# Kernel optimization log

Hardware: AMD Instinct MI355X
Metric: run time of the kernel (lower is better)

The kernel has to match this reference:

```python
import jax, jax.numpy as jnp
import numpy as np

H, C = 5, 128          # heads, hidden_channels
NUM_GRAPHS = 500
N_NODES, N_EDGES = 20000, 320000


def gat_layer(x, edge_attr, src, dst, W, We, a_src, a_dst, a_edge, b):
    """PyG GATConv with edge_dim, add_self_loops=True, fill_value='mean', concat heads."""
    N = x.shape[0]
    ed = edge_attr.dtype
    # self-loop edge_attr = scatter-mean of incoming edge_attr per target node
    deg = jax.ops.segment_sum(jnp.ones((dst.shape[0],), ed), dst, num_segments=N)
    loop_attr = jax.ops.segment_sum(edge_attr, dst, num_segments=N) / jnp.maximum(deg, 1.0)[:, None]
    loop = jnp.arange(N, dtype=src.dtype)
    s = jnp.concatenate([src, loop])
    d = jnp.concatenate([dst, loop])
    ea = jnp.concatenate([edge_attr, loop_attr], axis=0)
    h = (x @ W).reshape(N, H, C)            # [N,H,C]
    e = (ea @ We).reshape(-1, H, C)         # [E2,H,C]
    a_l = (h * a_src).sum(-1)               # [N,H]
    a_r = (h * a_dst).sum(-1)               # [N,H]
    a_e = (e * a_edge).sum(-1)              # [E2,H]
    alpha = jax.nn.leaky_relu(a_l[s] + a_r[d] + a_e, 0.2)
    # segment softmax over destination neighborhoods
    amax = jax.ops.segment_max(alpha, d, num_segments=N)
    ex = jnp.exp(alpha - amax[d])
    denom = jax.ops.segment_sum(ex, d, num_segments=N)
    att = ex / (denom[d] + 1e-16)           # [E2,H]
    msg = h[s] * att[..., None]             # [E2,H,C]
    out = jax.ops.segment_sum(msg, d, num_segments=N).reshape(N, H * C)
    return out + b


def setup_inputs() -> dict:
    key = jax.random.key(0)
    ks = jax.random.split(key, 24)
    p = lambda k, sh: (jax.random.normal(k, sh, dtype=jnp.float32) * 0.05)
    inp = {
        "x": jax.random.normal(ks[0], (N_NODES, 43), dtype=jnp.float32),
        "edge_attr": jax.random.normal(ks[1], (N_EDGES, 10), dtype=jnp.float32),
        "W1": p(ks[2], (43, H * C)),   "We1": p(ks[3], (10, H * C)),
        "asrc1": p(ks[4], (H, C)), "adst1": p(ks[5], (H, C)), "aedge1": p(ks[6], (H, C)),
        "b1": jnp.zeros((H * C,), jnp.float32),
        "W2": p(ks[7], (H * C, H * C)), "We2": p(ks[8], (10, H * C)),
        "asrc2": p(ks[9], (H, C)), "adst2": p(ks[10], (H, C)), "aedge2": p(ks[11], (H, C)),
        "b2": jnp.zeros((H * C,), jnp.float32),
        "W3": p(ks[12], (H * C, H * C)), "We3": p(ks[13], (10, H * C)),
        "asrc3": p(ks[14], (H, C)), "adst3": p(ks[15], (H, C)), "aedge3": p(ks[16], (H, C)),
        "b3": jnp.zeros((H * C,), jnp.float32),
        "Wlin": p(ks[17], (H * C, 1)), "blin": jnp.zeros((1,), jnp.float32),
        "edge_index": jax.random.randint(ks[18], (2, N_EDGES), 0, N_NODES, dtype=jnp.int32),
        "batch": jnp.sort(jax.random.randint(ks[19], (N_NODES,), 0, NUM_GRAPHS, dtype=jnp.int32)),
    }
    return inp


def reference(x, edge_attr, W1, We1, asrc1, adst1, aedge1, b1,
              W2, We2, asrc2, adst2, aedge2, b2,
              W3, We3, asrc3, adst3, aedge3, b3,
              Wlin, blin, edge_index, batch):
    src, dst = edge_index[0], edge_index[1]
    h = jax.nn.relu(gat_layer(x, edge_attr, src, dst, W1, We1, asrc1, adst1, aedge1, b1))
    h = jax.nn.relu(gat_layer(h, edge_attr, src, dst, W2, We2, asrc2, adst2, aedge2, b2))
    h = gat_layer(h, edge_attr, src, dst, W3, We3, asrc3, adst3, aedge3, b3)
    # global mean pool over graphs
    cnt = jax.ops.segment_sum(jnp.ones((h.shape[0],), h.dtype), batch, num_segments=NUM_GRAPHS)
    pooled = jax.ops.segment_sum(h, batch, num_segments=NUM_GRAPHS) / jnp.maximum(cnt, 1.0)[:, None]
    return (pooled @ Wlin + blin).squeeze(-1)   # [NUM_GRAPHS]
```

## Files before the change

kernel.cpp:

```cpp
#include <hip/hip_runtime.h>

#define N_NODESC 20000
#define N_EDGESC 320000
#define HC 640
#define NGRAPH 500

typedef unsigned short u16;
typedef unsigned int u32;
typedef __attribute__((ext_vector_type(8))) short bf16x8;
typedef __attribute__((ext_vector_type(4))) float f32x4;

__device__ __forceinline__ float wred_sum(float v){
  #pragma unroll
  for(int o=32;o;o>>=1) v += __shfl_xor(v,o,64);
  return v;
}
__device__ __forceinline__ float lrelu(float x){ return x>0.f? x:0.2f*x; }

__device__ __forceinline__ u16 f2bf(float f){
  u32 u=__float_as_uint(f);
  u32 r=u+0x7FFFu+((u>>16)&1u);
  return (u16)(r>>16);
}
__device__ __forceinline__ float bf2f(u16 s){ return __uint_as_float(((u32)s)<<16); }
__device__ __forceinline__ float bflo(u32 w){ return __uint_as_float(w<<16); }
__device__ __forceinline__ float bfhi(u32 w){ return __uint_as_float(w&0xFFFF0000u); }

__device__ __forceinline__ void gload16(const void* g, void* l){
  __builtin_amdgcn_global_load_lds((const __attribute__((address_space(1))) void*)g,
                                   (__attribute__((address_space(3))) void*)l, 16, 0, 0);
}

__device__ __forceinline__ size_t fidx(int r, int k, int KB){
  return ((size_t)(r>>4)*KB + (k>>5))*512 + (((k>>3)&3)*16 + (r&15))*8 + (k&7);
}


__global__ void k_count(const int* __restrict__ dst, int* __restrict__ cnt){
  int i=blockIdx.x*blockDim.x+threadIdx.x;
  if(i>=N_EDGESC) return;
  atomicAdd(&cnt[dst[i]],1);
}

__global__ void k_scan(const int* __restrict__ cnt, int* __restrict__ rptr, int* __restrict__ pos){
  __shared__ int ps[1024];
  int t=threadIdx.x;
  const int CH=20;
  int beg=t*CH, end=min(beg+CH, N_NODESC);
  int s=0;
  for(int i=beg;i<end;i++) s+=cnt[i];
  ps[t]=s; __syncthreads();
  for(int off=1;off<1024;off<<=1){
    int v=(t>=off)? ps[t-off]:0;
    __syncthreads();
    ps[t]+=v;
    __syncthreads();
  }
  int base=ps[t]-s;
  for(int i=beg;i<end;i++){ rptr[i]=base; pos[i]=base; base+=cnt[i]; }
}

__global__ void k_scatter(const int* __restrict__ dst, const int* __restrict__ src,
                          const float* __restrict__ eattr, int* __restrict__ pos,
                          int* __restrict__ srcE, int* __restrict__ dstC,
                          float* __restrict__ eattrC){
  int i=blockIdx.x*blockDim.x+threadIdx.x;
  if(i>=N_EDGESC) return;
  int d=dst[i];
  int j=atomicAdd(&pos[d],1);
  dstC[j]=d;
  srcE[j]=src[i];
  const float* ep=&eattr[(size_t)i*10];
  float* op=&eattrC[(size_t)j*10];
  #pragma unroll
  for(int k=0;k<10;k++) op[k]=ep[k];
}

__global__ __launch_bounds__(256) void k_loop_attr(const float* __restrict__ eattrC,
    const int* __restrict__ rptr, const int* __restrict__ cnt,
    float* __restrict__ lattr){
  int tid=threadIdx.x, lane=tid&63;
  int n=blockIdx.x*4+(tid>>6);
  if(n>=N_NODESC) return;
  int beg=rptr[n], deg=cnt[n];
  float s[10]={0,0,0,0,0,0,0,0,0,0};
  for(int off=lane; off<deg; off+=64){
    const float* ep=&eattrC[(size_t)(beg+off)*10];
    #pragma unroll
    for(int k=0;k<10;k++) s[k]+=ep[k];
  }
  float inv=1.f/fmaxf((float)deg,1.f);
  #pragma unroll
  for(int k=0;k<10;k++){
    float tot=wred_sum(s[k]);
    if(lane==0) lattr[(size_t)n*10+k]=tot*inv;
  }
}


__global__ void k_padxb(const float* __restrict__ x, u16* __restrict__ xb){
  int idx=blockIdx.x*blockDim.x+threadIdx.x;
  if(idx>=N_NODESC*64) return;
  int n=idx>>6, kk=idx&63;
  float v = kk<43 ? x[n*43+kk] : 0.f;
  xb[idx]=f2bf(v);
}

__global__ void k_conv_w3(const float* __restrict__ W0, const float* __restrict__ W1,
                          const float* __restrict__ W2,
                          u16* __restrict__ hi, u16* __restrict__ lo){
  const int R0=HC*64, R1=R0+HC*HC;
  const int TOT=R1+HC*HC;
  int idx=blockIdx.x*blockDim.x+threadIdx.x;
  if(idx>=TOT) return;
  const float* W; int local, KP, KL, base;
  if(idx<R0){ W=W0; local=idx; KP=64; KL=43; base=0; }
  else if(idx<R1){ W=W1; local=idx-R0; KP=HC; KL=HC; base=R0; }
  else { W=W2; local=idx-R1; KP=HC; KL=HC; base=R1; }
  int n=local/KP, kk=local-n*KP;
  float v = kk<KL ? W[(size_t)kk*HC+n] : 0.f;
  u16 h=f2bf(v);
  size_t off=(size_t)base + fidx(n,kk,KP>>5);
  hi[off]=h;
  lo[off]=f2bf(v-bf2f(h));
}


__global__ void k_ve3(const float* __restrict__ We0, const float* __restrict__ ae0,
                      const float* __restrict__ We1, const float* __restrict__ ae1,
                      const float* __restrict__ We2, const float* __restrict__ ae2,
                      float* __restrict__ ve3){
  int t=threadIdx.x;
  if(t>=150) return;
  int L=t/50, r=t-50*L, k=r/5, h=r%5;
  const float* We = (L==0)?We0:(L==1)?We1:We2;
  const float* ae = (L==0)?ae0:(L==1)?ae1:ae2;
  float s=0.f;
  for(int c=0;c<128;c++) s += We[k*HC + h*128 + c]*ae[h*128+c];
  ve3[t]=s;
}

__global__ void k_vs0(const float* __restrict__ W0, const float* __restrict__ asrc,
                      const float* __restrict__ adst,
                      const float* __restrict__ bias2, const float* __restrict__ wlin,
                      float* __restrict__ VS, float* __restrict__ VD,
                      float* __restrict__ cb){
  int t=threadIdx.x;
  if(t<320){
    int k=t/5, h=t%5;
    float sv=0.f, dv=0.f;
    if(k<43){
      for(int c=0;c<128;c++){
        float wv=W0[(size_t)k*HC + h*128 + c];
        sv+=wv*asrc[h*128+c];
        dv+=wv*adst[h*128+c];
      }
    }
    VS[t]=sv; VD[t]=dv;
  }else{
    int lane=t-320;
    float s=0.f;
    for(int c=lane;c<HC;c+=64) s+=bias2[c]*wlin[c];
    s=wred_sum(s);
    if(lane==0) cb[0]=s;
  }
}

__global__ void k_vq2(const float* __restrict__ W2, const float* __restrict__ asrc,
                      const float* __restrict__ adst, const float* __restrict__ wlin,
                      float* __restrict__ V2){
  int t=blockIdx.x*blockDim.x+threadIdx.x;
  if(t>=HC*15) return;
  int k=t/15, o=t-15*k;
  int h=o%5, grp=o/5;
  const float* v = (grp==0)? asrc : (grp==1)? adst : wlin;
  const float* wr=&W2[(size_t)k*HC + h*128];
  const float* vr=&v[h*128];
  float s=0.f;
  for(int c=0;c<128;c++) s+=wr[c]*vr[c];
  V2[t]=s;
}

__global__ __launch_bounds__(256) void k_alar0(const float* __restrict__ x,
    const float* __restrict__ VS, const float* __restrict__ VD,
    float* __restrict__ al, float* __restrict__ ar){
  __shared__ float vs[320], vd[320];
  if(threadIdx.x<320){ vs[threadIdx.x]=VS[threadIdx.x]; vd[threadIdx.x]=VD[threadIdx.x]; }
  __syncthreads();
  int idx=blockIdx.x*blockDim.x+threadIdx.x;
  if(idx>=N_NODESC*5) return;
  int n=idx/5, h=idx-5*n;
  float sa=0.f, sd=0.f;
  const float* xr=&x[(size_t)n*43];
  for(int k=0;k<43;k++){
    float xv=xr[k];
    sa+=xv*vs[k*5+h];
    sd+=xv*vd[k*5+h];
  }
  al[idx]=sa; ar[idx]=sd;
}

__global__ __launch_bounds__(256) void k_edge_terms3(const float* __restrict__ eattrC,
    const float* __restrict__ lattr, const float* __restrict__ ve3,
    float* __restrict__ aeC3, float* __restrict__ ael3){
  __shared__ float ves[150];
  if(threadIdx.x<150) ves[threadIdx.x]=ve3[threadIdx.x];
  __syncthreads();
  const int NEDGET=N_EDGESC+N_NODESC*5;
  int idx=blockIdx.x*blockDim.x+threadIdx.x;
  if(idx>=3*NEDGET) return;
  int L=idx/NEDGET, r=idx-L*NEDGET;
  const float* vl=&ves[L*50];
  if(r<N_EDGESC){
    float ev[10];
    const float* ep=&eattrC[(size_t)r*10];
    #pragma unroll
    for(int k=0;k<10;k++) ev[k]=ep[k];
    #pragma unroll
    for(int hh=0;hh<5;hh++){
      float s=0.f;
      #pragma unroll
      for(int k=0;k<10;k++) s+=ev[k]*vl[k*5+hh];
      aeC3[(size_t)L*N_EDGESC*5 + (size_t)r*5+hh]=s;
    }
  }else{
    int t=r-N_EDGESC;
    int n=t/5, h=t-5*n;
    float s=0.f;
    #pragma unroll
    for(int k=0;k<10;k++) s+=lattr[(size_t)n*10+k]*vl[k*5+h];
    ael3[(size_t)L*N_NODESC*5 + t]=s;
  }
}

__global__ void k_edgew(const int* __restrict__ srcE, const int* __restrict__ dstC,
                        const float* __restrict__ al, const float* __restrict__ ar,
                        const float* __restrict__ aeC, float* __restrict__ wE){
  int j=blockIdx.x*blockDim.x+threadIdx.x;
  if(j>=N_EDGESC) return;
  int s=srcE[j], d=dstC[j];
  const float* av=&aeC[(size_t)j*5];
  float* wp=&wE[(size_t)j*5];
  #pragma unroll
  for(int h=0;h<5;h++)
    wp[h]=__expf(lrelu(al[s*5+h]+ar[d*5+h]+av[h]));
}


__global__ __launch_bounds__(256) void k_aggx(const u16* __restrict__ xb,
    const int* __restrict__ srcE, const int* __restrict__ rptr, const int* __restrict__ cnt,
    const float* __restrict__ al, const float* __restrict__ ar, const float* __restrict__ ael,
    const float* __restrict__ wE,
    u16* __restrict__ aggx, float* __restrict__ den0){
  const size_t HSZ=(size_t)N_NODESC*64;
  int tid=threadIdx.x, lane=tid&63;
  int n=blockIdx.x*4+(tid>>6);
  if(n>=N_NODESC) return;
  float den[5], acc[5];
  #pragma unroll
  for(int h=0;h<5;h++)
    den[h]=__expf(lrelu(al[n*5+h]+ar[n*5+h]+ael[n*5+h]));
  float xn=bf2f(xb[(size_t)n*64+lane]);
  #pragma unroll
  for(int h=0;h<5;h++) acc[h]=den[h]*xn;
  int beg=rptr[n], end=beg+cnt[n];
  int j=beg;
  for(; j+7<end; j+=8){
    int sj[8]; float xv[8];
    #pragma unroll
    for(int u=0;u<8;u++) sj[u]=srcE[j+u];
    #pragma unroll
    for(int u=0;u<8;u++) xv[u]=bf2f(xb[(size_t)sj[u]*64+lane]);
    #pragma unroll
    for(int u=0;u<8;u++){
      const float* wp=&wE[(size_t)(j+u)*5];
      #pragma unroll
      for(int h=0;h<5;h++){
        float w=wp[h];
        den[h]+=w;
        acc[h]+=w*xv[u];
      }
    }
  }
  for(; j<end; j++){
    int sj=srcE[j];
    float xv=bf2f(xb[(size_t)sj*64+lane]);
    const float* wp=&wE[(size_t)j*5];
    #pragma unroll
    for(int h=0;h<5;h++){
      float w=wp[h];
      den[h]+=w;
      acc[h]+=w*xv;
    }
  }
  size_t fo=fidx(n,lane,2);
  #pragma unroll
  for(int h=0;h<5;h++) aggx[(size_t)h*HSZ+fo]=f2bf(acc[h]);
  if(lane<5) den0[(size_t)n*5+lane]=den[lane];
}

__global__ __launch_bounds__(256,3) void k_gemm_l0b(
    const u16* __restrict__ AGX,
    const u16* __restrict__ Bhi, const u16* __restrict__ Blo,
    const float* __restrict__ den0, const float* __restrict__ bias,
    u16* __restrict__ A1, int M, int nblk){
  const size_t HSZ=(size_t)N_NODESC*64;
  __shared__ u16 lds[2*3*4096];
  int tid=threadIdx.x;
  int lane=tid&63;
  int w=tid>>6;
  int l15=lane&15, lg=lane>>4;
  int orig=blockIdx.x;
  int q=nblk>>3, r=nblk&7;
  int xcd=orig&7, off=orig>>3;
  int wg=(xcd<r? xcd*(q+1) : r*(q+1)+(xcd-r)*q)+off;
  int by=wg/5, bx=wg-5*by;
  int row0=by*128, col0=bx*128;
  int wr=w>>1, wc=w&1;
  const u16* A=AGX+(size_t)bx*HSZ;

  f32x4 zero = {0.f,0.f,0.f,0.f};
  f32x4 acc[4][4];
  #pragma unroll
  for(int i=0;i<4;i++)
    #pragma unroll
    for(int j=0;j<4;j++) acc[i][j]=zero;

  auto stage=[&](int b, int k0){
    u16* base = lds + b*3*4096;
    int kb=k0>>5;
    #pragma unroll
    for(int c=0;c<2;c++){
      int sb=w+4*c;
      size_t af=((size_t)((row0>>4)+sb)*2 + kb)*512 + lane*8;
      size_t bf=((size_t)((col0>>4)+sb)*2 + kb)*512 + lane*8;
      gload16(A+af, base + sb*512);
      gload16(Bhi+bf, base+4096 + sb*512);
      gload16(Blo+bf, base+8192 + sb*512);
    }
  };

  stage(0,0);
  __syncthreads();
  int cur=0;
  for(int t=0;t<2;t++){
    if(t==0) stage(1,32);
    u16* cb = lds + cur*3*4096;
    bf16x8 ah[4], bh[4], bl[4];
    #pragma unroll
    for(int i=0;i<4;i++){
      ah[i]=*(const bf16x8*)&cb[(wr*4+i)*512 + lane*8];
      bh[i]=*(const bf16x8*)&cb[4096+(wc*4+i)*512 + lane*8];
      bl[i]=*(const bf16x8*)&cb[8192+(wc*4+i)*512 + lane*8];
    }
    #pragma unroll
    for(int i=0;i<4;i++)
      #pragma unroll
      for(int j=0;j<4;j++){
        acc[i][j]=__builtin_amdgcn_mfma_f32_16x16x32_bf16(ah[i],bh[j],acc[i][j],0,0,0);
        acc[i][j]=__builtin_amdgcn_mfma_f32_16x16x32_bf16(ah[i],bl[j],acc[i][j],0,0,0);
      }
    __syncthreads();
    cur^=1;
  }

  #pragma unroll
  for(int i=0;i<4;i++){
    #pragma unroll
    for(int j=0;j<4;j++){
      int col=col0+wc*64+j*16+l15;
      float bv=bias[col];
      #pragma unroll
      for(int rr=0;rr<4;rr++){
        int row=row0+wr*64+i*16+lg*4+rr;
        if(row<M){
          float dv=den0[(size_t)row*5+bx];
          float v=acc[i][j][rr]/(dv+1e-16f)+bv;
          v=fmaxf(v,0.f);
          A1[fidx(row,col,20)]=f2bf(v);
        }
      }
    }
  }
}


__global__ __launch_bounds__(256,3) void k_gemm64(
    const u16* __restrict__ A,
    const u16* __restrict__ B,
    const float* __restrict__ asrc, const float* __restrict__ adst,
    u16* __restrict__ hb, float* __restrict__ al, float* __restrict__ ar,
    int M, int KP, int nblk){
  __shared__ u16 lds[4*6144];
  int tid=threadIdx.x;
  int lane=tid&63;
  int w=tid>>6;
  int l15=lane&15, lg=lane>>4;
  int orig=blockIdx.x;
  int q=nblk>>3, r=nblk&7;
  int xcd=orig&7, off=orig>>3;
  int wg=(xcd<r? xcd*(q+1) : r*(q+1)+(xcd-r)*q)+off;
  int by=wg/5, bx=wg-5*by;
  int row0=by*64, col0=bx*128;
  int KB=KP>>5;

  f32x4 zero = {0.f,0.f,0.f,0.f};
  f32x4 acc[4][2];
  #pragma unroll
  for(int i=0;i<4;i++){ acc[i][0]=zero; acc[i][1]=zero; }

  auto stage=[&](int b, int k0){
    u16* base = lds + b*6144;
    int kb=k0>>5;
    size_t af=((size_t)((row0>>4)+w)*KB + kb)*512 + lane*8;
    gload16(A+af, base + w*512);
    #pragma unroll
    for(int c=0;c<2;c++){
      int sb=w+4*c;
      size_t bf=((size_t)((col0>>4)+sb)*KB + kb)*512 + lane*8;
      gload16(B+bf, base+2048 + sb*512);
    }
  };

  int nt=KP/32;
  stage(0,0);
  stage(1,32);
  for(int t=0;t<nt;t++){
    int nb=t+2;
    if(nb<nt) stage(nb&3, nb*32);
    if(nb<nt)      { asm volatile("s_waitcnt vmcnt(6)" ::: "memory"); }
    else if(t+1<nt){ asm volatile("s_waitcnt vmcnt(3)" ::: "memory"); }
    else           { asm volatile("s_waitcnt vmcnt(0)" ::: "memory"); }
    __builtin_amdgcn_sched_barrier(0);
    __builtin_amdgcn_s_barrier();
    u16* cb = lds + (t&3)*6144;
    bf16x8 ah[4], bh[2];
    #pragma unroll
    for(int i=0;i<4;i++) ah[i]=*(const bf16x8*)&cb[i*512 + lane*8];
    #pragma unroll
    for(int j=0;j<2;j++) bh[j]=*(const bf16x8*)&cb[2048+(w*2+j)*512 + lane*8];
    #pragma unroll
    for(int i=0;i<4;i++){
      acc[i][0]=__builtin_amdgcn_mfma_f32_16x16x32_bf16(ah[i],bh[0],acc[i][0],0,0,0);
      acc[i][1]=__builtin_amdgcn_mfma_f32_16x16x32_bf16(ah[i],bh[1],acc[i][1],0,0,0);
    }
  }
  __syncthreads();

  float asv[2], adv[2];
  #pragma unroll
  for(int j=0;j<2;j++){
    int c=col0+w*32+j*16+l15;
    asv[j]=asrc[c]; adv[j]=adst[c];
  }
  #pragma unroll
  for(int i=0;i<4;i++){
    #pragma unroll
    for(int j=0;j<2;j++){
      #pragma unroll
      for(int rr=0;rr<4;rr++){
        int row=row0+i*16+lg*4+rr;
        if(row<M)
          hb[(size_t)row*HC + ((w&1)*32+j*16+l15)*10 + bx*2+(w>>1)]=f2bf(acc[i][j][rr]);
      }
    }
  }
  float* redAl=(float*)lds;
  float* redAr=redAl+256;
  #pragma unroll
  for(int i=0;i<4;i++){
    #pragma unroll
    for(int rr=0;rr<4;rr++){
      float sa=0.f, sd=0.f;
      #pragma unroll
      for(int j=0;j<2;j++){
        sa+=acc[i][j][rr]*asv[j];
        sd+=acc[i][j][rr]*adv[j];
      }
      #pragma unroll
      for(int o=1;o<16;o<<=1){
        sa+=__shfl_xor(sa,o,64); sd+=__shfl_xor(sd,o,64);
      }
      if(l15==0){
        int lr=i*16+lg*4+rr;
        redAl[lr*4+w]=sa; redAr[lr*4+w]=sd;
      }
    }
  }
  __syncthreads();
  if(tid<64){
    int row=row0+tid;
    if(row<M){
      al[(size_t)row*5+bx]=redAl[tid*4]+redAl[tid*4+1]+redAl[tid*4+2]+redAl[tid*4+3];
      ar[(size_t)row*5+bx]=redAr[tid*4]+redAr[tid*4+1]+redAr[tid*4+2]+redAr[tid*4+3];
    }
  }
}

__global__ __launch_bounds__(256) void k_qal2(const u16* __restrict__ A2,
    const float* __restrict__ V2,
    float* __restrict__ al, float* __restrict__ ar, float* __restrict__ qn){
  __shared__ float Vs[HC*15];
  __shared__ float red[4][16][15];
  int tid=threadIdx.x, lane=tid&63, w=tid>>6;
  for(int i=tid;i<HC*15;i+=256) Vs[i]=V2[i];
  __syncthreads();
  int nb=blockIdx.x;
  int koct=lane>>4;
  float acc[15];
  #pragma unroll
  for(int o=0;o<15;o++) acc[o]=0.f;
  for(int kb=w*5; kb<w*5+5; kb++){
    bf16x8 v=*(const bf16x8*)&A2[((size_t)nb*20+kb)*512 + (size_t)lane*8];
    #pragma unroll
    for(int e=0;e<8;e++){
      float xv=bf2f((u16)v[e]);
      int k=kb*32+koct*8+e;
      const float* vp=&Vs[k*15];
      #pragma unroll
      for(int o=0;o<15;o++) acc[o]+=xv*vp[o];
    }
  }
  #pragma unroll
  for(int o=0;o<15;o++){
    acc[o]+=__shfl_xor(acc[o],16,64);
    acc[o]+=__shfl_xor(acc[o],32,64);
  }
  if((lane&15)==lane){
    #pragma unroll
    for(int o=0;o<15;o++) red[w][lane][o]=acc[o];
  }
  __syncthreads();
  if(tid<240){
    int node=tid/15, o=tid-15*node;
    float s=red[0][node][o]+red[1][node][o]+red[2][node][o]+red[3][node][o];
    int n=nb*16+node;
    if(o<5)       al[(size_t)n*5+o]=s;
    else if(o<10) ar[(size_t)n*5+(o-5)]=s;
    else          qn[(size_t)n*5+(o-10)]=s;
  }
}

__global__ __launch_bounds__(256) void k_agg(const u16* __restrict__ hb, const int* __restrict__ srcE,
    const int* __restrict__ rptr, const int* __restrict__ cnt,
    const float* __restrict__ al, const float* __restrict__ ar, const float* __restrict__ ael,
    const float* __restrict__ wE, const float* __restrict__ bias,
    u16* __restrict__ ohi){
  int tid=threadIdx.x, lane=tid&63;
  int n=blockIdx.x*4+(tid>>6);
  if(n>=N_NODESC) return;
  float den[5], acc[10];
  #pragma unroll
  for(int h=0;h<5;h++)
    den[h]=__expf(lrelu(al[n*5+h]+ar[n*5+h]+ael[n*5+h]));
  {
    const u32* sp=(const u32*)(hb+(size_t)n*HC+lane*10);
    #pragma unroll
    for(int j2=0;j2<5;j2++){
      u32 wv=sp[j2];
      acc[2*j2]  =den[j2]*bflo(wv);
      acc[2*j2+1]=den[j2]*bfhi(wv);
    }
  }
  int beg=rptr[n], end=beg+cnt[n];
  int j=beg;
  for(; j+3<end; j+=4){
    int sj[4];
    #pragma unroll
    for(int u=0;u<4;u++) sj[u]=srcE[j+u];
    float w[4][5];
    #pragma unroll
    for(int u=0;u<4;u++){
      const float* wp=&wE[(size_t)(j+u)*5];
      #pragma unroll
      for(int h=0;h<5;h++) w[u][h]=wp[h];
    }
    u32 wv[4][5];
    #pragma unroll
    for(int u=0;u<4;u++){
      const u32* hr=(const u32*)(hb+(size_t)sj[u]*HC+lane*10);
      #pragma unroll
      for(int j2=0;j2<5;j2++) wv[u][j2]=hr[j2];
    }
    #pragma unroll
    for(int u=0;u<4;u++){
      #pragma unroll
      for(int j2=0;j2<5;j2++){
        den[j2]+=w[u][j2];
        acc[2*j2]  +=w[u][j2]*bflo(wv[u][j2]);
        acc[2*j2+1]+=w[u][j2]*bfhi(wv[u][j2]);
      }
    }
  }
  for(; j<end; j++){
    int sj=srcE[j];
    const float* wp=&wE[(size_t)j*5];
    float w[5];
    #pragma unroll
    for(int h=0;h<5;h++){ w[h]=wp[h]; den[h]+=w[h]; }
    const u32* hr=(const u32*)(hb+(size_t)sj*HC+lane*10);
    #pragma unroll
    for(int j2=0;j2<5;j2++){
      u32 wv=hr[j2];
      acc[2*j2]  +=w[j2]*bflo(wv);
      acc[2*j2+1]+=w[j2]*bfhi(wv);
    }
  }
  #pragma unroll
  for(int k=0;k<10;k++){
    int ccol=lane+64*k;
    float vv=acc[k]/(den[k>>1]+1e-16f)+bias[ccol];
    vv=fmaxf(vv,0.f);
    ohi[fidx(n,ccol,20)]=f2bf(vv);
  }
}

__global__ __launch_bounds__(256) void k_agg_last(const float* __restrict__ qn,
    const int* __restrict__ srcE, const int* __restrict__ rptr, const int* __restrict__ cnt,
    const float* __restrict__ al, const float* __restrict__ ar, const float* __restrict__ ael,
    const float* __restrict__ aeC, const float* __restrict__ cb,
    float* __restrict__ pnode){
  int tid=threadIdx.x;
  int sub=tid&15;
  int n=blockIdx.x*16+(tid>>4);
  if(n>=N_NODESC) return;
  float arn[5], den[5], qs[5];
  #pragma unroll
  for(int h=0;h<5;h++) arn[h]=ar[n*5+h];
  #pragma unroll
  for(int h=0;h<5;h++){ den[h]=0.f; qs[h]=0.f; }
  if(sub==0){
    #pragma unroll
    for(int h=0;h<5;h++){
      float pp=__expf(lrelu(al[n*5+h]+arn[h]+ael[n*5+h]));
      den[h]=pp; qs[h]=pp*qn[(size_t)n*5+h];
    }
  }
  int beg=rptr[n], deg=cnt[n];
  for(int off=sub; off<deg; off+=16){
    int j=beg+off;
    int s=srcE[j];
    const float* av=&aeC[(size_t)j*5];
    const float* qv=&qn[(size_t)s*5];
    #pragma unroll
    for(int h=0;h<5;h++){
      float pp=__expf(lrelu(al[s*5+h]+arn[h]+av[h]));
      den[h]+=pp; qs[h]+=pp*qv[h];
    }
  }
  #pragma unroll
  for(int h=0;h<5;h++){
    #pragma unroll
    for(int o=1;o<16;o<<=1){
      den[h]+=__shfl_xor(den[h],o,16);
      qs[h]+=__shfl_xor(qs[h],o,16);
    }
  }
  if(sub==0){
    float s=0.f;
    #pragma unroll
    for(int h=0;h<5;h++) s+=qs[h]/(den[h]+1e-16f);
    pnode[n]=s+cb[0];
  }
}

__global__ __launch_bounds__(256) void k_graphout(const float* __restrict__ pnode,
    const int* __restrict__ batch, const float* __restrict__ blin,
    float* __restrict__ out){
  int tid=threadIdx.x, lane=tid&63;
  int g=blockIdx.x*4+(tid>>6);
  if(g>=NGRAPH) return;
  auto lb=[&](int val){
    int lo=0, hi=N_NODESC;
    while(lo<hi){ int mid=(lo+hi)>>1; if(batch[mid]<val) lo=mid+1; else hi=mid; }
    return lo;
  };
  int s0=lb(g), s1=lb(g+1);
  float s=0.f;
  for(int i=s0+lane;i<s1;i+=64) s+=pnode[i];
  s=wred_sum(s);
  if(lane==0) out[g]=s/fmaxf((float)(s1-s0),1.f)+blin[0];
}


extern "C" void kernel_launch(void* const* d_in, const int* in_sizes, int n_in,
                              void* d_out, int out_size, void* d_ws, size_t ws_size,
                              hipStream_t stream){
  const float* x     = (const float*)d_in[0];
  const float* eattr = (const float*)d_in[1];
  const float* W[3]    ={(const float*)d_in[2],(const float*)d_in[8],(const float*)d_in[14]};
  const float* We[3]   ={(const float*)d_in[3],(const float*)d_in[9],(const float*)d_in[15]};
  const float* asrc[3] ={(const float*)d_in[4],(const float*)d_in[10],(const float*)d_in[16]};
  const float* adst[3] ={(const float*)d_in[5],(const float*)d_in[11],(const float*)d_in[17]};
  const float* aedge[3]={(const float*)d_in[6],(const float*)d_in[12],(const float*)d_in[18]};
  const float* bias[3] ={(const float*)d_in[7],(const float*)d_in[13],(const float*)d_in[19]};
  const float* Wlin  = (const float*)d_in[20];
  const float* blin  = (const float*)d_in[21];
  const int* eind    = (const int*)d_in[22];
  const int* srcp    = eind;
  const int* dstp    = eind + N_EDGESC;
  const int* batch   = (const int*)d_in[23];
  float* out = (float*)d_out;

  char* ws=(char*)d_ws;
  size_t o=0;
  auto alloc=[&](size_t bytes)->void*{ void* p=ws+o; o=(o+bytes+255)&~(size_t)255; return p; };
  u16* hb   =(u16*)alloc((size_t)N_NODESC*HC*2);
  u16* Ahi =(u16*)alloc((size_t)N_NODESC*HC*2);
  u16* xb  =(u16*)alloc((size_t)N_NODESC*64*2);
  u16* aggx=(u16*)alloc((size_t)5*N_NODESC*64*2);
  const int WB0=0, WB1=HC*64, WB2=WB1+HC*HC;
  u16* Bthi3=(u16*)alloc((size_t)(WB2+HC*HC)*2);
  u16* Btlo3=(u16*)alloc((size_t)(WB2+HC*HC)*2);
  float* al   =(float*)alloc((size_t)N_NODESC*5*4);
  float* ar   =(float*)alloc((size_t)N_NODESC*5*4);
  float* qn   =(float*)alloc((size_t)N_NODESC*5*4);
  float* den0 =(float*)alloc((size_t)N_NODESC*5*4);
  float* ael3 =(float*)alloc((size_t)3*N_NODESC*5*4);
  float* aeC3 =(float*)alloc((size_t)3*N_EDGESC*5*4);
  float* wE   =(float*)alloc((size_t)N_EDGESC*5*4);
  float* lattr=(float*)alloc((size_t)N_NODESC*10*4);
  float* eattrC=(float*)alloc((size_t)N_EDGESC*10*4);
  float* ve3  =(float*)alloc(256*4);
  float* VS0  =(float*)alloc(320*4);
  float* VD0  =(float*)alloc(320*4);
  float* V2   =(float*)alloc((size_t)HC*15*4);
  float* cbv  =(float*)alloc(64*4);
  float* pnode=(float*)alloc((size_t)N_NODESC*4);
  int* cntI   =(int*)alloc((size_t)N_NODESC*4);
  int* rptr   =(int*)alloc((size_t)N_NODESC*4);
  int* pos    =(int*)alloc((size_t)N_NODESC*4);
  int* srcE   =(int*)alloc((size_t)N_EDGESC*4);
  int* dstC   =(int*)alloc((size_t)N_EDGESC*4);

  hipMemsetAsync(cntI,0,(size_t)N_NODESC*4,stream);

  k_count<<<(N_EDGESC+255)/256,256,0,stream>>>(dstp,cntI);
  k_scan<<<1,1024,0,stream>>>(cntI,rptr,pos);
  k_scatter<<<(N_EDGESC+255)/256,256,0,stream>>>(dstp,srcp,eattr,pos,srcE,dstC,eattrC);
  k_loop_attr<<<(N_NODESC+3)/4,256,0,stream>>>(eattrC,rptr,cntI,lattr);
  k_padxb<<<(N_NODESC*64+255)/256,256,0,stream>>>(x,xb);
  k_ve3<<<1,256,0,stream>>>(We[0],aedge[0],We[1],aedge[1],We[2],aedge[2],ve3);
  k_vs0<<<1,384,0,stream>>>(W[0],asrc[0],adst[0],bias[2],Wlin,VS0,VD0,cbv);
  k_vq2<<<(HC*15+255)/256,256,0,stream>>>(W[2],asrc[2],adst[2],Wlin,V2);
  {
    int tot=WB2+HC*HC;
    k_conv_w3<<<(tot+255)/256,256,0,stream>>>(W[0],W[1],W[2],Bthi3,Btlo3);
  }
  {
    const int NEDGET=N_EDGESC+N_NODESC*5;
    k_edge_terms3<<<(3*NEDGET+255)/256,256,0,stream>>>(eattrC,lattr,ve3,aeC3,ael3);
  }
  k_alar0<<<(N_NODESC*5+255)/256,256,0,stream>>>(x,VS0,VD0,al,ar);

  const int NBLK0=5*((N_NODESC+127)/128);
  const int NBLK64=5*((N_NODESC+63)/64);

  k_edgew<<<(N_EDGESC+255)/256,256,0,stream>>>(srcE,dstC,al,ar,aeC3,wE);
  k_aggx<<<(N_NODESC+3)/4,256,0,stream>>>(xb,srcE,rptr,cntI,al,ar,ael3,wE,aggx,den0);
  k_gemm_l0b<<<NBLK0,256,0,stream>>>(aggx,Bthi3+WB0,Btlo3+WB0,den0,bias[0],Ahi,N_NODESC,NBLK0);

  {
    const float* aeL = aeC3 + (size_t)1*N_EDGESC*5;
    const float* aelL= ael3 + (size_t)1*N_NODESC*5;
    k_gemm64<<<NBLK64,256,0,stream>>>(Ahi,Bthi3+WB1,
        asrc[1],adst[1],hb,al,ar,N_NODESC,HC,NBLK64);
    k_edgew<<<(N_EDGESC+255)/256,256,0,stream>>>(srcE,dstC,al,ar,aeL,wE);
    k_agg<<<(N_NODESC+3)/4,256,0,stream>>>(hb,srcE,rptr,cntI,al,ar,aelL,wE,bias[1],Ahi);
  }
  {
    const float* aelL= ael3 + (size_t)2*N_NODESC*5;
    k_qal2<<<N_NODESC/16,256,0,stream>>>(Ahi,V2,al,ar,qn);
    k_agg_last<<<(N_NODESC+15)/16,256,0,stream>>>(qn,srcE,rptr,cntI,al,ar,aelL,aeC3+(size_t)2*N_EDGESC*5,cbv,pnode);
  }
  k_graphout<<<(NGRAPH+3)/4,256,0,stream>>>(pnode,batch,blin,out);
}
```

Baseline: 371.9 us.

## Fuse layer-2 projection into aggregation and layer-0 edge weights into edge terms

The layer-2 aggregation kernel now projects its relu output straight onto the 15 attention/readout vectors with a wave-wide shuffle reduction, writing al2/ar2/qn. This drops the bf16 hidden-state write and the separate k_qal2 pass. Separately, k_alar0 is moved ahead of k_edge_terms3, and the layer-0 edge slice now computes exp(lrelu(...)) edge weights directly, removing one k_edgew launch and the aeC3 layer-0 round trip. The cost is 15 shuffle reductions per node, uncoalesced V2 reads per lane, and extra gathers inside the edge-terms kernel.

```diff
diff --git a/kernel.cpp b/kernel.cpp
--- a/kernel.cpp
+++ b/kernel.cpp
@@ -202,7 +202,9 @@
 
 __global__ __launch_bounds__(256) void k_edge_terms3(const float* __restrict__ eattrC,
     const float* __restrict__ lattr, const float* __restrict__ ve3,
-    float* __restrict__ aeC3, float* __restrict__ ael3){
+    const int* __restrict__ srcE, const int* __restrict__ dstC,
+    const float* __restrict__ al0, const float* __restrict__ ar0,
+    float* __restrict__ aeC3, float* __restrict__ ael3, float* __restrict__ wE0){
   __shared__ float ves[150];
   if(threadIdx.x<150) ves[threadIdx.x]=ve3[threadIdx.x];
   __syncthreads();
@@ -216,12 +218,23 @@
     const float* ep=&eattrC[(size_t)r*10];
     #pragma unroll
     for(int k=0;k<10;k++) ev[k]=ep[k];
-    #pragma unroll
-    for(int hh=0;hh<5;hh++){
-      float s=0.f;
-      #pragma unroll
-      for(int k=0;k<10;k++) s+=ev[k]*vl[k*5+hh];
-      aeC3[(size_t)L*N_EDGESC*5 + (size_t)r*5+hh]=s;
+    if(L==0){
+      int s=srcE[r], d=dstC[r];
+      #pragma unroll
+      for(int hh=0;hh<5;hh++){
+        float sum=0.f;
+        #pragma unroll
+        for(int k=0;k<10;k++) sum+=ev[k]*vl[k*5+hh];
+        wE0[(size_t)r*5+hh]=__expf(lrelu(al0[s*5+hh]+ar0[d*5+hh]+sum));
+      }
+    }else{
+      #pragma unroll
+      for(int hh=0;hh<5;hh++){
+        float sum=0.f;
+        #pragma unroll
+        for(int k=0;k<10;k++) sum+=ev[k]*vl[k*5+hh];
+        aeC3[(size_t)L*N_EDGESC*5 + (size_t)r*5+hh]=sum;
+      }
     }
   }else{
     int t=r-N_EDGESC;
@@ -497,55 +510,12 @@
   }
 }
 
-__global__ __launch_bounds__(256) void k_qal2(const u16* __restrict__ A2,
-    const float* __restrict__ V2,
-    float* __restrict__ al, float* __restrict__ ar, float* __restrict__ qn){
-  __shared__ float Vs[HC*15];
-  __shared__ float red[4][16][15];
-  int tid=threadIdx.x, lane=tid&63, w=tid>>6;
-  for(int i=tid;i<HC*15;i+=256) Vs[i]=V2[i];
-  __syncthreads();
-  int nb=blockIdx.x;
-  int koct=lane>>4;
-  float acc[15];
-  #pragma unroll
-  for(int o=0;o<15;o++) acc[o]=0.f;
-  for(int kb=w*5; kb<w*5+5; kb++){
-    bf16x8 v=*(const bf16x8*)&A2[((size_t)nb*20+kb)*512 + (size_t)lane*8];
-    #pragma unroll
-    for(int e=0;e<8;e++){
-      float xv=bf2f((u16)v[e]);
-      int k=kb*32+koct*8+e;
-      const float* vp=&Vs[k*15];
-      #pragma unroll
-      for(int o=0;o<15;o++) acc[o]+=xv*vp[o];
-    }
-  }
-  #pragma unroll
-  for(int o=0;o<15;o++){
-    acc[o]+=__shfl_xor(acc[o],16,64);
-    acc[o]+=__shfl_xor(acc[o],32,64);
-  }
-  if((lane&15)==lane){
-    #pragma unroll
-    for(int o=0;o<15;o++) red[w][lane][o]=acc[o];
-  }
-  __syncthreads();
-  if(tid<240){
-    int node=tid/15, o=tid-15*node;
-    float s=red[0][node][o]+red[1][node][o]+red[2][node][o]+red[3][node][o];
-    int n=nb*16+node;
-    if(o<5)       al[(size_t)n*5+o]=s;
-    else if(o<10) ar[(size_t)n*5+(o-5)]=s;
-    else          qn[(size_t)n*5+(o-10)]=s;
-  }
-}
-
 __global__ __launch_bounds__(256) void k_agg(const u16* __restrict__ hb, const int* __restrict__ srcE,
     const int* __restrict__ rptr, const int* __restrict__ cnt,
     const float* __restrict__ al, const float* __restrict__ ar, const float* __restrict__ ael,
     const float* __restrict__ wE, const float* __restrict__ bias,
-    u16* __restrict__ ohi){
+    const float* __restrict__ V2,
+    float* __restrict__ al2, float* __restrict__ ar2, float* __restrict__ qn){
   int tid=threadIdx.x, lane=tid&63;
   int n=blockIdx.x*4+(tid>>6);
   if(n>=N_NODESC) return;
@@ -606,12 +576,30 @@
       acc[2*j2+1]+=w[j2]*bfhi(wv);
     }
   }
+  float facc[15];
+  #pragma unroll
+  for(int o=0;o<15;o++) facc[o]=0.f;
   #pragma unroll
   for(int k=0;k<10;k++){
     int ccol=lane+64*k;
     float vv=acc[k]/(den[k>>1]+1e-16f)+bias[ccol];
     vv=fmaxf(vv,0.f);
-    ohi[fidx(n,ccol,20)]=f2bf(vv);
+    const float* vp=&V2[(size_t)ccol*15];
+    #pragma unroll
+    for(int o=0;o<15;o++) facc[o]+=vv*vp[o];
+  }
+  #pragma unroll
+  for(int o=0;o<15;o++){
+    #pragma unroll
+    for(int st=1;st<64;st<<=1) facc[o]+=__shfl_xor(facc[o],st,64);
+  }
+  if(lane==0){
+    #pragma unroll
+    for(int h=0;h<5;h++){
+      al2[(size_t)n*5+h]=facc[h];
+      ar2[(size_t)n*5+h]=facc[5+h];
+      qn [(size_t)n*5+h]=facc[10+h];
+    }
   }
 }
 
@@ -714,6 +702,8 @@
   u16* Btlo3=(u16*)alloc((size_t)(WB2+HC*HC)*2);
   float* al   =(float*)alloc((size_t)N_NODESC*5*4);
   float* ar   =(float*)alloc((size_t)N_NODESC*5*4);
+  float* al2  =(float*)alloc((size_t)N_NODESC*5*4);
+  float* ar2  =(float*)alloc((size_t)N_NODESC*5*4);
   float* qn   =(float*)alloc((size_t)N_NODESC*5*4);
   float* den0 =(float*)alloc((size_t)N_NODESC*5*4);
   float* ael3 =(float*)alloc((size_t)3*N_NODESC*5*4);
@@ -747,16 +737,15 @@
     int tot=WB2+HC*HC;
     k_conv_w3<<<(tot+255)/256,256,0,stream>>>(W[0],W[1],W[2],Bthi3,Btlo3);
   }
+  k_alar0<<<(N_NODESC*5+255)/256,256,0,stream>>>(x,VS0,VD0,al,ar);
   {
     const int NEDGET=N_EDGESC+N_NODESC*5;
-    k_edge_terms3<<<(3*NEDGET+255)/256,256,0,stream>>>(eattrC,lattr,ve3,aeC3,ael3);
-  }
-  k_alar0<<<(N_NODESC*5+255)/256,256,0,stream>>>(x,VS0,VD0,al,ar);
+    k_edge_terms3<<<(3*NEDGET+255)/256,256,0,stream>>>(eattrC,lattr,ve3,srcE,dstC,al,ar,aeC3,ael3,wE);
+  }
 
   const int NBLK0=5*((N_NODESC+127)/128);
   const int NBLK64=5*((N_NODESC+63)/64);
 
-  k_edgew<<<(N_EDGESC+255)/256,256,0,stream>>>(srcE,dstC,al,ar,aeC3,wE);
   k_aggx<<<(N_NODESC+3)/4,256,0,stream>>>(xb,srcE,rptr,cntI,al,ar,ael3,wE,aggx,den0);
   k_gemm_l0b<<<NBLK0,256,0,stream>>>(aggx,Bthi3+WB0,Btlo3+WB0,den0,bias[0],Ahi,N_NODESC,NBLK0);
 
@@ -766,12 +755,11 @@
     k_gemm64<<<NBLK64,256,0,stream>>>(Ahi,Bthi3+WB1,
         asrc[1],adst[1],hb,al,ar,N_NODESC,HC,NBLK64);
     k_edgew<<<(N_EDGESC+255)/256,256,0,stream>>>(srcE,dstC,al,ar,aeL,wE);
-    k_agg<<<(N_NODESC+3)/4,256,0,stream>>>(hb,srcE,rptr,cntI,al,ar,aelL,wE,bias[1],Ahi);
+    k_agg<<<(N_NODESC+3)/4,256,0,stream>>>(hb,srcE,rptr,cntI,al,ar,aelL,wE,bias[1],V2,al2,ar2,qn);
   }
   {
     const float* aelL= ael3 + (size_t)2*N_NODESC*5;
-    k_qal2<<<N_NODESC/16,256,0,stream>>>(Ahi,V2,al,ar,qn);
-    k_agg_last<<<(N_NODESC+15)/16,256,0,stream>>>(qn,srcE,rptr,cntI,al,ar,aelL,aeC3+(size_t)2*N_EDGESC*5,cbv,pnode);
+    k_agg_last<<<(N_NODESC+15)/16,256,0,stream>>>(qn,srcE,rptr,cntI,al2,ar2,aelL,aeC3+(size_t)2*N_EDGESC*5,cbv,pnode);
   }
   k_graphout<<<(NGRAPH+3)/4,256,0,stream>>>(pnode,batch,blin,out);
 }
```

New measurement: 388.1 us. 4.4% more time.
